# Kernel tuning notes

Hardware: AMD Instinct MI355X
Metric: run time of the kernel (lower is better)

## Reference

```python
import jax, jax.numpy as jnp
import numpy as np

BATCH = 4096
TEMP = 0.5
EPS = 1e-12  # torch F.normalize eps

def setup_inputs() -> dict:
    key = jax.random.key(0)
    k1, k2 = jax.random.split(key)
    z_i = jax.random.normal(k1, (BATCH, 256), dtype=jnp.float32)
    z_j = jax.random.normal(k2, (BATCH, 256), dtype=jnp.float32)
    return {"z_i": z_i, "z_j": z_j}

def _l2norm(x):
    n = jnp.sqrt(jnp.sum(x * x, axis=1, keepdims=True))
    return x / jnp.maximum(n, EPS)

def reference(z_i, z_j):
    B = z_i.shape[0]
    zi = _l2norm(z_i)
    zj = _l2norm(z_j)
    reps = jnp.concatenate([zi, zj], axis=0)          # [2B, D]
    # rows are unit-norm, so cosine similarity == dot product (GEMM)
    sim = reps @ reps.T                                # [2B, 2B]
    sim_ij = jnp.diagonal(sim, offset=B)               # [B]
    sim_ji = jnp.diagonal(sim, offset=-B)              # [B]
    positives = jnp.concatenate([sim_ij, sim_ji], 0)   # [2B]
    nominator = jnp.exp(positives / TEMP)
    # negatives_mask: ones with the two same-view BxB diagonal blocks zeroed
    idx = jnp.arange(2 * B)
    half = (idx >= B).astype(sim.dtype)                # 0 for first half, 1 for second
    mask = (half[:, None] != half[None, :]).astype(sim.dtype)  # cross-view blocks = 1
    denom = jnp.sum(mask * jnp.exp(sim / TEMP), axis=1)
    loss_partial = -jnp.log(nominator / denom)
    return jnp.sum(loss_partial) / (2 * B)
```

## Files before the change

### kernel.cpp

```cpp
#include <hip/hip_runtime.h>
#include <hip/hip_bf16.h>

#define BATCH 4096
#define DIM 256

typedef __attribute__((ext_vector_type(8))) short short8;
typedef __attribute__((ext_vector_type(4))) float f32x4;

__device__ inline unsigned short f2bf(float f) {
    union { float f; unsigned u; } x; x.f = f;
    unsigned r = x.u + 0x7fffu + ((x.u >> 16) & 1u);
    return (unsigned short)(r >> 16);
}

#define WS_FAST_BYTES ((size_t)4 * 1024 * 1024 + 3 * 4096 * sizeof(float) + 64)

__device__ inline short8* lds8(unsigned short* base, int r, int c) {
    int byte = (r << 7) + (c << 1);
    byte ^= (r & 7) << 4;
    return reinterpret_cast<short8*>(reinterpret_cast<char*>(base) + byte);
}

__global__ __launch_bounds__(256) void norm2_kernel(
    const float* __restrict__ zi, const float* __restrict__ zj,
    unsigned short* __restrict__ zib, unsigned short* __restrict__ zjb,
    float* __restrict__ pos, float* __restrict__ rowsum, float* __restrict__ colsum) {
    const int tid = threadIdx.x;
    if (blockIdx.x < 16) rowsum[blockIdx.x * 256 + tid] = 0.f;
    else if (blockIdx.x < 32) colsum[(blockIdx.x - 16) * 256 + tid] = 0.f;

    const int wid  = tid >> 6;
    const int lane = tid & 63;
    const int row  = blockIdx.x * 4 + wid;
    const float4 vi = reinterpret_cast<const float4*>(zi)[row * 64 + lane];
    const float4 vj = reinterpret_cast<const float4*>(zj)[row * 64 + lane];
    float si = vi.x * vi.x + vi.y * vi.y + vi.z * vi.z + vi.w * vi.w;
    float sj = vj.x * vj.x + vj.y * vj.y + vj.z * vj.z + vj.w * vj.w;
    float d  = vi.x * vj.x + vi.y * vj.y + vi.z * vj.z + vi.w * vj.w;
#pragma unroll
    for (int o = 1; o < 64; o <<= 1) {
        si += __shfl_xor(si, o);
        sj += __shfl_xor(sj, o);
        d  += __shfl_xor(d, o);
    }
    const float ii = 1.0f / fmaxf(sqrtf(si), 1e-12f);
    const float ij = 1.0f / fmaxf(sqrtf(sj), 1e-12f);
    ushort4 a = make_ushort4(f2bf(vi.x * ii), f2bf(vi.y * ii), f2bf(vi.z * ii), f2bf(vi.w * ii));
    ushort4 b = make_ushort4(f2bf(vj.x * ij), f2bf(vj.y * ij), f2bf(vj.z * ij), f2bf(vj.w * ij));
    reinterpret_cast<ushort4*>(zib)[row * 64 + lane] = a;
    reinterpret_cast<ushort4*>(zjb)[row * 64 + lane] = b;
    if (lane == 0) pos[row] = d * ii * ij;
}

__global__ __launch_bounds__(256) void sim128_kernel(
    const unsigned short* __restrict__ zib, const unsigned short* __restrict__ zjb,
    float* __restrict__ rowsum, float* __restrict__ colsum) {
    __shared__ unsigned short As[2][128 * 64];
    __shared__ unsigned short Bs[2][128 * 64];
    const int bi = blockIdx.x, bj = blockIdx.y;
    const int tid  = threadIdx.x;
    const int wave = tid >> 6;
    const int lane = tid & 63;
    const int wr = (wave >> 1) << 6;
    const int wc = (wave & 1) << 6;
    const int fr = lane & 15;
    const int ko = (lane >> 4) << 3;

    const unsigned short* gA = zib + (size_t)bi * 128 * DIM;
    const unsigned short* gB = zjb + (size_t)bj * 128 * DIM;
    int rr[4], cc[4];
#pragma unroll
    for (int i = 0; i < 4; ++i) {
        int chunk = i * 256 + tid;
        rr[i] = chunk >> 3;
        cc[i] = (chunk & 7) << 3;
    }

    short8 pa[4], pb[4];
#pragma unroll
    for (int i = 0; i < 4; ++i) {
        pa[i] = *reinterpret_cast<const short8*>(gA + rr[i] * DIM + cc[i]);
        pb[i] = *reinterpret_cast<const short8*>(gB + rr[i] * DIM + cc[i]);
    }
#pragma unroll
    for (int i = 0; i < 4; ++i) {
        *lds8(As[0], rr[i], cc[i]) = pa[i];
        *lds8(Bs[0], rr[i], cc[i]) = pb[i];
    }

    f32x4 acc[4][4] = {};

#pragma unroll
    for (int s = 0; s < 4; ++s) {
        const int cur = s & 1;
        __syncthreads();
        if (s < 3) {
#pragma unroll
            for (int i = 0; i < 4; ++i) {
                pa[i] = *reinterpret_cast<const short8*>(gA + rr[i] * DIM + (s + 1) * 64 + cc[i]);
                pb[i] = *reinterpret_cast<const short8*>(gB + rr[i] * DIM + (s + 1) * 64 + cc[i]);
            }
        }
#pragma unroll
        for (int kk = 0; kk < 2; ++kk) {
            int c = kk * 32 + ko;
            short8 a0 = *lds8(As[cur], wr +      fr, c);
            short8 a1 = *lds8(As[cur], wr + 16 + fr, c);
            short8 a2 = *lds8(As[cur], wr + 32 + fr, c);
            short8 a3 = *lds8(As[cur], wr + 48 + fr, c);
            short8 b0 = *lds8(Bs[cur], wc +      fr, c);
            short8 b1 = *lds8(Bs[cur], wc + 16 + fr, c);
            short8 b2 = *lds8(Bs[cur], wc + 32 + fr, c);
            short8 b3 = *lds8(Bs[cur], wc + 48 + fr, c);
            acc[0][0] = __builtin_amdgcn_mfma_f32_16x16x32_bf16(a0, b0, acc[0][0], 0, 0, 0);
            acc[0][1] = __builtin_amdgcn_mfma_f32_16x16x32_bf16(a0, b1, acc[0][1], 0, 0, 0);
            acc[0][2] = __builtin_amdgcn_mfma_f32_16x16x32_bf16(a0, b2, acc[0][2], 0, 0, 0);
            acc[0][3] = __builtin_amdgcn_mfma_f32_16x16x32_bf16(a0, b3, acc[0][3], 0, 0, 0);
            acc[1][0] = __builtin_amdgcn_mfma_f32_16x16x32_bf16(a1, b0, acc[1][0], 0, 0, 0);
            acc[1][1] = __builtin_amdgcn_mfma_f32_16x16x32_bf16(a1, b1, acc[1][1], 0, 0, 0);
            acc[1][2] = __builtin_amdgcn_mfma_f32_16x16x32_bf16(a1, b2, acc[1][2], 0, 0, 0);
            acc[1][3] = __builtin_amdgcn_mfma_f32_16x16x32_bf16(a1, b3, acc[1][3], 0, 0, 0);
            acc[2][0] = __builtin_amdgcn_mfma_f32_16x16x32_bf16(a2, b0, acc[2][0], 0, 0, 0);
            acc[2][1] = __builtin_amdgcn_mfma_f32_16x16x32_bf16(a2, b1, acc[2][1], 0, 0, 0);
            acc[2][2] = __builtin_amdgcn_mfma_f32_16x16x32_bf16(a2, b2, acc[2][2], 0, 0, 0);
            acc[2][3] = __builtin_amdgcn_mfma_f32_16x16x32_bf16(a2, b3, acc[2][3], 0, 0, 0);
            acc[3][0] = __builtin_amdgcn_mfma_f32_16x16x32_bf16(a3, b0, acc[3][0], 0, 0, 0);
            acc[3][1] = __builtin_amdgcn_mfma_f32_16x16x32_bf16(a3, b1, acc[3][1], 0, 0, 0);
            acc[3][2] = __builtin_amdgcn_mfma_f32_16x16x32_bf16(a3, b2, acc[3][2], 0, 0, 0);
            acc[3][3] = __builtin_amdgcn_mfma_f32_16x16x32_bf16(a3, b3, acc[3][3], 0, 0, 0);
        }
        if (s < 3) {
#pragma unroll
            for (int i = 0; i < 4; ++i) {
                *lds8(As[cur ^ 1], rr[i], cc[i]) = pa[i];
                *lds8(Bs[cur ^ 1], rr[i], cc[i]) = pb[i];
            }
        }
    }

    const float SC = 2.0f * 1.44269504088896f;
    float rs[4][4];
#pragma unroll
    for (int m = 0; m < 4; ++m)
#pragma unroll
        for (int r = 0; r < 4; ++r) rs[m][r] = 0.f;
    float cs[4] = {0.f, 0.f, 0.f, 0.f};
#pragma unroll
    for (int m = 0; m < 4; ++m)
#pragma unroll
        for (int n = 0; n < 4; ++n)
#pragma unroll
            for (int r = 0; r < 4; ++r) {
                float e = exp2f(acc[m][n][r] * SC);
                rs[m][r] += e;
                cs[n] += e;
            }

#pragma unroll
    for (int m = 0; m < 4; ++m)
#pragma unroll
        for (int r = 0; r < 4; ++r) {
            float v = rs[m][r];
            v += __shfl_xor(v, 1); v += __shfl_xor(v, 2);
            v += __shfl_xor(v, 4); v += __shfl_xor(v, 8);
            if ((lane & 15) == 0) {
                int row = bi * 128 + wr + m * 16 + (lane >> 4) * 4 + r;
                atomicAdd(&rowsum[row], v);
            }
        }
#pragma unroll
    for (int n = 0; n < 4; ++n) {
        float v = cs[n];
        v += __shfl_xor(v, 16); v += __shfl_xor(v, 32);
        if (lane < 16) atomicAdd(&colsum[bj * 128 + wc + n * 16 + lane], v);
    }
}

__global__ __launch_bounds__(256) void loss_kernel(
    const float* __restrict__ rowsum, const float* __restrict__ colsum,
    const float* __restrict__ pos, float* __restrict__ out) {
    float a = 0.f;
    for (int i = threadIdx.x; i < BATCH; i += 256)
        a += __logf(rowsum[i]) + __logf(colsum[i]) - 4.0f * pos[i];
#pragma unroll
    for (int o = 1; o < 64; o <<= 1) a += __shfl_xor(a, o);
    __shared__ float red[4];
    if ((threadIdx.x & 63) == 0) red[threadIdx.x >> 6] = a;
    __syncthreads();
    if (threadIdx.x == 0) {
        float t = red[0] + red[1] + red[2] + red[3];
        out[0] = t * (1.0f / (2.0f * BATCH));
    }
}

__device__ inline short8* ldsp128(unsigned short* base, int r, int c) {
    int byte = (r << 8) + (c << 1);
    byte ^= (r & 7) << 4;
    return reinterpret_cast<short8*>(reinterpret_cast<char*>(base) + byte);
}

__global__ __launch_bounds__(256) void init_kernel(float* __restrict__ rowsum,
                                                   float* __restrict__ colsum) {
    int i = blockIdx.x * 256 + threadIdx.x;
    rowsum[i] = 0.f;
    colsum[i] = 0.f;
}

__global__ __launch_bounds__(256) void norm_kernel(
    const float* __restrict__ zi, const float* __restrict__ zj,
    float* __restrict__ ninv_i, float* __restrict__ ninv_j, float* __restrict__ pos) {
    const int wid  = threadIdx.x >> 6;
    const int lane = threadIdx.x & 63;
    const int row  = blockIdx.x * 4 + wid;
    const float4 vi = reinterpret_cast<const float4*>(zi)[row * 64 + lane];
    const float4 vj = reinterpret_cast<const float4*>(zj)[row * 64 + lane];
    float si = vi.x * vi.x + vi.y * vi.y + vi.z * vi.z + vi.w * vi.w;
    float sj = vj.x * vj.x + vj.y * vj.y + vj.z * vj.z + vj.w * vj.w;
    float d  = vi.x * vj.x + vi.y * vj.y + vi.z * vj.z + vi.w * vj.w;
#pragma unroll
    for (int o = 1; o < 64; o <<= 1) {
        si += __shfl_xor(si, o);
        sj += __shfl_xor(sj, o);
        d  += __shfl_xor(d, o);
    }
    if (lane == 0) {
        float ii = 1.0f / fmaxf(sqrtf(si), 1e-12f);
        float ij = 1.0f / fmaxf(sqrtf(sj), 1e-12f);
        ninv_i[row] = ii;
        ninv_j[row] = ij;
        pos[row] = d * ii * ij;
    }
}

__global__ __launch_bounds__(256) void sim_kernel(
    const float* __restrict__ zi, const float* __restrict__ zj,
    const float* __restrict__ ninv_i, const float* __restrict__ ninv_j,
    float* __restrict__ rowsum, float* __restrict__ colsum) {
    __shared__ unsigned short As[64 * 128];
    __shared__ unsigned short Bs[64 * 128];
    const int bi = blockIdx.x, bj = blockIdx.y;
    const int tid  = threadIdx.x;
    const int wave = tid >> 6;
    const int lane = tid & 63;
    const int wr = (wave >> 1) << 5;
    const int wc = (wave & 1) << 5;
    const int fr = lane & 15;
    const int ko = (lane >> 4) << 3;

    f32x4 acc[2][2] = {};

    for (int h = 0; h < 2; ++h) {
#pragma unroll
        for (int it = 0; it < 4; ++it) {
            int chunk = tid + it * 256;
            int r = chunk >> 4;
            int c = (chunk & 15) << 3;
            int ga = bi * 64 + r;
            int gb = bj * 64 + r;
            int cgl = h * 128 + c;
            const float4* pa = reinterpret_cast<const float4*>(zi) + ga * 64 + (cgl >> 2);
            const float4* pb = reinterpret_cast<const float4*>(zj) + gb * 64 + (cgl >> 2);
            float4 a0 = pa[0], a1 = pa[1];
            float4 b0 = pb[0], b1 = pb[1];
            float ia = ninv_i[ga];
            float ib = ninv_j[gb];
            short8 va, vb;
            va[0] = (short)f2bf(a0.x * ia); va[1] = (short)f2bf(a0.y * ia);
            va[2] = (short)f2bf(a0.z * ia); va[3] = (short)f2bf(a0.w * ia);
            va[4] = (short)f2bf(a1.x * ia); va[5] = (short)f2bf(a1.y * ia);
            va[6] = (short)f2bf(a1.z * ia); va[7] = (short)f2bf(a1.w * ia);
            vb[0] = (short)f2bf(b0.x * ib); vb[1] = (short)f2bf(b0.y * ib);
            vb[2] = (short)f2bf(b0.z * ib); vb[3] = (short)f2bf(b0.w * ib);
            vb[4] = (short)f2bf(b1.x * ib); vb[5] = (short)f2bf(b1.y * ib);
            vb[6] = (short)f2bf(b1.z * ib); vb[7] = (short)f2bf(b1.w * ib);
            *ldsp128(As, r, c) = va;
            *ldsp128(Bs, r, c) = vb;
        }
        __syncthreads();
#pragma unroll
        for (int kk = 0; kk < 4; ++kk) {
            int c = kk * 32 + ko;
            short8 a0 = *ldsp128(As, wr + fr, c);
            short8 a1 = *ldsp128(As, wr + 16 + fr, c);
            short8 b0 = *ldsp128(Bs, wc + fr, c);
            short8 b1 = *ldsp128(Bs, wc + 16 + fr, c);
            acc[0][0] = __builtin_amdgcn_mfma_f32_16x16x32_bf16(a0, b0, acc[0][0], 0, 0, 0);
            acc[0][1] = __builtin_amdgcn_mfma_f32_16x16x32_bf16(a0, b1, acc[0][1], 0, 0, 0);
            acc[1][0] = __builtin_amdgcn_mfma_f32_16x16x32_bf16(a1, b0, acc[1][0], 0, 0, 0);
            acc[1][1] = __builtin_amdgcn_mfma_f32_16x16x32_bf16(a1, b1, acc[1][1], 0, 0, 0);
        }
        __syncthreads();
    }

    const float SC = 2.0f * 1.44269504088896f;
    float rs[2][4];
#pragma unroll
    for (int m = 0; m < 2; ++m)
#pragma unroll
        for (int r = 0; r < 4; ++r) rs[m][r] = 0.f;
    float cs[2] = {0.f, 0.f};
#pragma unroll
    for (int m = 0; m < 2; ++m)
#pragma unroll
        for (int n = 0; n < 2; ++n)
#pragma unroll
            for (int r = 0; r < 4; ++r) {
                float e = exp2f(acc[m][n][r] * SC);
                rs[m][r] += e;
                cs[n] += e;
            }
#pragma unroll
    for (int m = 0; m < 2; ++m)
#pragma unroll
        for (int r = 0; r < 4; ++r) {
            float v = rs[m][r];
            v += __shfl_xor(v, 1); v += __shfl_xor(v, 2);
            v += __shfl_xor(v, 4); v += __shfl_xor(v, 8);
            if ((lane & 15) == 0) {
                int row = bi * 64 + wr + m * 16 + (lane >> 4) * 4 + r;
                atomicAdd(&rowsum[row], v);
            }
        }
#pragma unroll
    for (int n = 0; n < 2; ++n) {
        float v = cs[n];
        v += __shfl_xor(v, 16); v += __shfl_xor(v, 32);
        if (lane < 16) atomicAdd(&colsum[bj * 64 + wc + n * 16 + lane], v);
    }
}

extern "C" void kernel_launch(void* const* d_in, const int* in_sizes, int n_in,
                              void* d_out, int out_size, void* d_ws, size_t ws_size,
                              hipStream_t stream) {
    const float* zi = (const float*)d_in[0];
    const float* zj = (const float*)d_in[1];
    char* ws = (char*)d_ws;

    if (ws_size >= WS_FAST_BYTES) {
        unsigned short* zib = (unsigned short*)ws;
        unsigned short* zjb = (unsigned short*)(ws + (size_t)2 * 1024 * 1024);
        float* pos    = (float*)(ws + (size_t)4 * 1024 * 1024);
        float* rowsum = pos + 4096;
        float* colsum = rowsum + 4096;
        norm2_kernel<<<BATCH / 4, 256, 0, stream>>>(zi, zj, zib, zjb, pos, rowsum, colsum);
        dim3 grid(32, 32);
        sim128_kernel<<<grid, 256, 0, stream>>>(zib, zjb, rowsum, colsum);
        loss_kernel<<<1, 256, 0, stream>>>(rowsum, colsum, pos, (float*)d_out);
    } else {
        float* wsf = (float*)ws;
        float* ninv_i = wsf;
        float* ninv_j = wsf + 4096;
        float* pos    = wsf + 8192;
        float* rowsum = wsf + 12288;
        float* colsum = wsf + 16384;
        init_kernel<<<16, 256, 0, stream>>>(rowsum, colsum);
        norm_kernel<<<BATCH / 4, 256, 0, stream>>>(zi, zj, ninv_i, ninv_j, pos);
        dim3 grid(64, 64);
        sim_kernel<<<grid, 256, 0, stream>>>(zi, zj, ninv_i, ninv_j, rowsum, colsum);
        loss_kernel<<<1, 256, 0, stream>>>(rowsum, colsum, pos, (float*)d_out);
    }
}
```

Measured before the change: 36.67 us.

## Parallelize loss reduction across blocks and remap sim tile order for L2 locality

Replaces the single-block final loss reduction with a 32-block kernel. Each block reduces a slice, atomically accumulates into a workspace scalar, and the last block (found via an atomic counter) writes the output. It also remaps the sim128 workgroup index so that consecutive workgroups share B tiles and spread across XCDs, for better cache reuse. The price is extra atomics and a last-block pattern, plus the tmp and counter values that must be reset in the norm kernel.

```diff
diff --git a/kernel.cpp b/kernel.cpp
--- a/kernel.cpp
+++ b/kernel.cpp
@@ -24,10 +24,12 @@
 __global__ __launch_bounds__(256) void norm2_kernel(
     const float* __restrict__ zi, const float* __restrict__ zj,
     unsigned short* __restrict__ zib, unsigned short* __restrict__ zjb,
-    float* __restrict__ pos, float* __restrict__ rowsum, float* __restrict__ colsum) {
+    float* __restrict__ pos, float* __restrict__ rowsum, float* __restrict__ colsum,
+    float* __restrict__ tmp, int* __restrict__ counter) {
     const int tid = threadIdx.x;
     if (blockIdx.x < 16) rowsum[blockIdx.x * 256 + tid] = 0.f;
     else if (blockIdx.x < 32) colsum[(blockIdx.x - 16) * 256 + tid] = 0.f;
+    else if (blockIdx.x == 32 && tid == 0) { tmp[0] = 0.f; *counter = 0; }
 
     const int wid  = tid >> 6;
     const int lane = tid & 63;
@@ -57,7 +59,9 @@
     float* __restrict__ rowsum, float* __restrict__ colsum) {
     __shared__ unsigned short As[2][128 * 64];
     __shared__ unsigned short Bs[2][128 * 64];
-    const int bi = blockIdx.x, bj = blockIdx.y;
+    const int wg = blockIdx.x + (blockIdx.y << 5);
+    const int bi = ((wg & 7) << 2) + ((wg >> 3) & 3);
+    const int bj = wg >> 5;
     const int tid  = threadIdx.x;
     const int wave = tid >> 6;
     const int lane = tid & 63;
@@ -176,20 +180,29 @@
     }
 }
 
-__global__ __launch_bounds__(256) void loss_kernel(
+__global__ __launch_bounds__(256) void loss2_kernel(
     const float* __restrict__ rowsum, const float* __restrict__ colsum,
-    const float* __restrict__ pos, float* __restrict__ out) {
-    float a = 0.f;
-    for (int i = threadIdx.x; i < BATCH; i += 256)
-        a += __logf(rowsum[i]) + __logf(colsum[i]) - 4.0f * pos[i];
+    const float* __restrict__ pos, float* __restrict__ tmp,
+    int* __restrict__ counter, float* __restrict__ out) {
+    const int b = blockIdx.x;
+    const int tid = threadIdx.x;
+    const int idx = (b & 15) * 256 + tid;
+    float a = (b < 16) ? (__logf(rowsum[idx]) - 4.0f * pos[idx])
+                       : __logf(colsum[idx]);
 #pragma unroll
     for (int o = 1; o < 64; o <<= 1) a += __shfl_xor(a, o);
     __shared__ float red[4];
-    if ((threadIdx.x & 63) == 0) red[threadIdx.x >> 6] = a;
+    if ((tid & 63) == 0) red[tid >> 6] = a;
     __syncthreads();
-    if (threadIdx.x == 0) {
-        float t = red[0] + red[1] + red[2] + red[3];
-        out[0] = t * (1.0f / (2.0f * BATCH));
+    if (tid == 0) {
+        float p = red[0] + red[1] + red[2] + red[3];
+        atomicAdd(tmp, p);
+        __threadfence();
+        int t = atomicAdd(counter, 1);
+        if (t == 31) {
+            float tot = atomicAdd(tmp, 0.0f);
+            out[0] = tot * (1.0f / (2.0f * BATCH));
+        }
     }
 }
 
@@ -329,6 +342,23 @@
     }
 }
 
+__global__ __launch_bounds__(256) void loss_kernel(
+    const float* __restrict__ rowsum, const float* __restrict__ colsum,
+    const float* __restrict__ pos, float* __restrict__ out) {
+    float a = 0.f;
+    for (int i = threadIdx.x; i < BATCH; i += 256)
+        a += __logf(rowsum[i]) + __logf(colsum[i]) - 4.0f * pos[i];
+#pragma unroll
+    for (int o = 1; o < 64; o <<= 1) a += __shfl_xor(a, o);
+    __shared__ float red[4];
+    if ((threadIdx.x & 63) == 0) red[threadIdx.x >> 6] = a;
+    __syncthreads();
+    if (threadIdx.x == 0) {
+        float t = red[0] + red[1] + red[2] + red[3];
+        out[0] = t * (1.0f / (2.0f * BATCH));
+    }
+}
+
 extern "C" void kernel_launch(void* const* d_in, const int* in_sizes, int n_in,
                               void* d_out, int out_size, void* d_ws, size_t ws_size,
                               hipStream_t stream) {
@@ -342,10 +372,12 @@
         float* pos    = (float*)(ws + (size_t)4 * 1024 * 1024);
         float* rowsum = pos + 4096;
         float* colsum = rowsum + 4096;
-        norm2_kernel<<<BATCH / 4, 256, 0, stream>>>(zi, zj, zib, zjb, pos, rowsum, colsum);
+        float* tmp    = colsum + 4096;
+        int*   counter = (int*)(tmp + 1);
+        norm2_kernel<<<BATCH / 4, 256, 0, stream>>>(zi, zj, zib, zjb, pos, rowsum, colsum, tmp, counter);
         dim3 grid(32, 32);
         sim128_kernel<<<grid, 256, 0, stream>>>(zib, zjb, rowsum, colsum);
-        loss_kernel<<<1, 256, 0, stream>>>(rowsum, colsum, pos, (float*)d_out);
+        loss2_kernel<<<32, 256, 0, stream>>>(rowsum, colsum, pos, tmp, counter, (float*)d_out);
     } else {
         float* wsf = (float*)ws;
         float* ninv_i = wsf;
```

Result: faster. 33.51 us (-8.6%).
